# Performance work log

Measured on AMD Instinct MI355X. Metric: run time of the kernel, lower is better.

The kernel has to match this reference:

```python
import jax, jax.numpy as jnp
import numpy as np

EMBED_DIM = 2048
NUM_HEAD = 32
NUM_GROUP = 8
B, S = 2, 2048


def setup_inputs() -> dict:
    key = jax.random.key(0)
    ks = jax.random.split(key, 9)
    D = EMBED_DIM // NUM_HEAD
    kv_dim = NUM_GROUP * D
    s = 0.02
    return {
        "x": jax.random.normal(ks[0], (B, S, EMBED_DIM), dtype=jnp.float32),
        "wq_w": jax.random.normal(ks[1], (EMBED_DIM, EMBED_DIM), dtype=jnp.float32) * s,
        "wq_b": jnp.zeros((EMBED_DIM,), dtype=jnp.float32),
        "wk_w": jax.random.normal(ks[2], (kv_dim, EMBED_DIM), dtype=jnp.float32) * s,
        "wk_b": jnp.zeros((kv_dim,), dtype=jnp.float32),
        "wv_w": jax.random.normal(ks[3], (kv_dim, EMBED_DIM), dtype=jnp.float32) * s,
        "wv_b": jnp.zeros((kv_dim,), dtype=jnp.float32),
        "out_w": jax.random.normal(ks[4], (EMBED_DIM, EMBED_DIM), dtype=jnp.float32) * s,
        "out_b": jnp.zeros((EMBED_DIM,), dtype=jnp.float32),
    }


def reference(x, wq_w, wq_b, wk_w, wk_b, wv_w, wv_b, out_w, out_b):
    b, s, e = x.shape
    H, G = NUM_HEAD, NUM_GROUP
    D = e // H
    r = H // G  # repeat_times
    # projections (torch Linear: x @ W.T + b)
    q = (x @ wq_w.T + wq_b).reshape(b, s, H, D)
    k = (x @ wk_w.T + wk_b).reshape(b, s, G, D)
    v = (x @ wv_w.T + wv_b).reshape(b, s, G, D)
    # faithful to torch.concat([data]*r, dim=2): TILE along head axis
    # (q-head h uses kv-head h mod G)
    k = jnp.concatenate([k] * r, axis=2)  # [b, s, H, D]
    v = jnp.concatenate([v] * r, axis=2)
    # [b, H, s_q, s_k]
    scores = jnp.einsum("bqhd,bkhd->bhqk", q, k) / (D ** 0.5)
    # faithful to F.softmax(dim=1): softmax over the HEAD axis
    attn = jax.nn.softmax(scores, axis=1)
    o = jnp.einsum("bhqk,bkhd->bqhd", attn, v).reshape(b, s, e)
    return o @ out_w.T + out_b
```

## Files before the change

### kernel.cpp

```cpp
#include <hip/hip_runtime.h>


typedef unsigned short u16;
typedef unsigned int u32;
typedef __attribute__((ext_vector_type(8))) __bf16 bf16x8;
typedef __attribute__((ext_vector_type(4))) float f32x4;
typedef __attribute__((ext_vector_type(4))) float float4_t;

#define GLD16(ldsp, gp)                                                  \
  __builtin_amdgcn_global_load_lds(                                      \
      (__attribute__((address_space(1))) void*)(void*)(gp),              \
      (__attribute__((address_space(3))) void*)(void*)(ldsp), 16, 0, 0)

static __device__ __forceinline__ u16 f2bf(float f) {
  union { float f; u32 u; } v; v.f = f;
  u32 u = v.u;
  u32 r = (u + 0x7fffu + ((u >> 16) & 1u)) >> 16;
  return (u16)r;
}

static __device__ __forceinline__ bf16x8 ld8(const u16* p) {
  return *(const bf16x8*)p;
}

#if __has_builtin(__builtin_amdgcn_exp2f)
static __device__ __forceinline__ float fexp2(float x) {
  return __builtin_amdgcn_exp2f(x);
}
#else
static __device__ __forceinline__ float fexp2(float x) {
  float r;
  asm("v_exp_f32 %0, %1\n\ts_nop 0" : "=v"(r) : "v"(x));
  return r;
}
#endif

static __device__ __forceinline__ u32 cvtpk(float a, float b) {
  u32 r;
  asm("v_cvt_pk_bf16_f32 %0, %1, %2" : "=v"(r) : "v"(a), "v"(b));
  return r;
}

static __device__ __forceinline__ void barrier_lgkm() {
  asm volatile("s_waitcnt lgkmcnt(0)" ::: "memory");
  __builtin_amdgcn_s_barrier();
  asm volatile("" ::: "memory");
}

static __device__ __forceinline__ float hsum4(float v) {
  v += __builtin_bit_cast(float, __builtin_amdgcn_update_dpp(
           0, __builtin_bit_cast(int, v), 0x124, 0xf, 0xf, true));
  v += __builtin_bit_cast(float, __builtin_amdgcn_update_dpp(
           0, __builtin_bit_cast(int, v), 0x128, 0xf, 0xf, true));
  return v;
}

__global__ void cvt_all(const float* __restrict__ x, const float* __restrict__ wq,
                        const float* __restrict__ wk, const float* __restrict__ wv,
                        const float* __restrict__ wo, u16* __restrict__ xb,
                        u16* __restrict__ wqb, u16* __restrict__ wkb,
                        u16* __restrict__ wvb, u16* __restrict__ wob) {
  int i = blockIdx.x * blockDim.x + threadIdx.x;
  const int stride = gridDim.x * blockDim.x;
  for (; i < 2359296; i += stride) {
    const float* src;
    u16* dst;
    int j;
    if (i < 1048576)      { src = x;  dst = xb;  j = i; }
    else if (i < 1572864) { src = wq; dst = wqb; j = i - 1048576; }
    else if (i < 1703936) { src = wk; dst = wkb; j = i - 1572864; }
    else if (i < 1835008) { src = wv; dst = wvb; j = i - 1703936; }
    else                  { src = wo; dst = wob; j = i - 1835008; }
    const float4_t* p = (const float4_t*)src + (size_t)j * 2;
    float4_t a = p[0], b = p[1];
    u32 w0 = (u32)f2bf(a[0]) | ((u32)f2bf(a[1]) << 16);
    u32 w1 = (u32)f2bf(a[2]) | ((u32)f2bf(a[3]) << 16);
    u32 w2 = (u32)f2bf(b[0]) | ((u32)f2bf(b[1]) << 16);
    u32 w3 = (u32)f2bf(b[2]) | ((u32)f2bf(b[3]) << 16);
    *(uint4*)(dst + (size_t)j * 8) = make_uint4(w0, w1, w2, w3);
  }
}

template <int MODE>
__global__ __launch_bounds__(256, 2)
void gemm_bt(const u16* __restrict__ A, const u16* __restrict__ Bw,
             const float* __restrict__ bias,
             u16* __restrict__ Cb, float* __restrict__ Cf, int N, float scale) {
  constexpr int K = 2048;
  constexpr int SHSZ = (MODE == 2) ? (128 * 136) : 8192;
  __shared__ u16 sh[SHSZ];
  u16* As = sh;
  u16* Bs = sh + 4096;
  const int tid = threadIdx.x;
  const int lane = tid & 63;
  const int w = tid >> 6;
  const int m0 = blockIdx.y * 128;
  const int n0 = blockIdx.x * 128;
  const int wr = (w >> 1) * 64, wc = (w & 1) * 64;
  const int r15 = lane & 15, kq = lane >> 4;

  f32x4 acc[4][4] = {};

  for (int k0 = 0; k0 < K; k0 += 32) {
#pragma unroll
    for (int i = 0; i < 2; ++i) {
      int c = i * 256 + tid;
      int r = c >> 2, ch = c & 3;
      int sc = (ch ^ (r & 3)) * 8;
      GLD16(&As[c * 8], &A[(size_t)(m0 + r) * K + k0 + sc]);
      GLD16(&Bs[c * 8], &Bw[(size_t)(n0 + r) * K + k0 + sc]);
    }
    __syncthreads();
    bf16x8 af[4], bfr[4];
#pragma unroll
    for (int mt = 0; mt < 4; ++mt) {
      int r = wr + mt * 16 + r15;
      af[mt] = ld8(&As[r * 32 + ((kq ^ (r15 & 3)) * 8)]);
    }
#pragma unroll
    for (int nt = 0; nt < 4; ++nt) {
      int r = wc + nt * 16 + r15;
      bfr[nt] = ld8(&Bs[r * 32 + ((kq ^ (r15 & 3)) * 8)]);
    }
#pragma unroll
    for (int mt = 0; mt < 4; ++mt)
#pragma unroll
      for (int nt = 0; nt < 4; ++nt)
        acc[mt][nt] = __builtin_amdgcn_mfma_f32_16x16x32_bf16(af[mt], bfr[nt], acc[mt][nt], 0, 0, 0);
    __syncthreads();
  }

  if constexpr (MODE == 2) {
#pragma unroll
    for (int mt = 0; mt < 4; ++mt)
#pragma unroll
      for (int nt = 0; nt < 4; ++nt) {
        int col = wc + nt * 16 + r15;
        float bv = bias[n0 + col];
#pragma unroll
        for (int r = 0; r < 4; ++r) {
          int row = wr + mt * 16 + kq * 4 + r;
          sh[col * 136 + row] = f2bf(acc[mt][nt][r] + bv);
        }
      }
    __syncthreads();
    const int m0l = m0 & 2047;
    const int bb = m0 >> 11;
#pragma unroll
    for (int i = 0; i < 8; ++i) {
      int c = i * 256 + tid;
      int cc = c >> 4, so = c & 15;
      int X = cc * 136 + (so >> 2) * 32 + (so & 3) * 4;
      u32 A0 = *(const u32*)&sh[X + 0];
      u32 A1 = *(const u32*)&sh[X + 2];
      u32 B0 = *(const u32*)&sh[X + 16];
      u32 B1 = *(const u32*)&sh[X + 18];
      u32 w0 = __builtin_amdgcn_perm(B0, A0, 0x05040100u);
      u32 w1 = __builtin_amdgcn_perm(B0, A0, 0x07060302u);
      u32 w2 = __builtin_amdgcn_perm(B1, A1, 0x05040100u);
      u32 w3 = __builtin_amdgcn_perm(B1, A1, 0x07060302u);
      *(uint4*)&Cb[(size_t)(bb * 512 + n0 + cc) * 2048 + m0l + so * 8] =
          make_uint4(w0, w1, w2, w3);
    }
  } else {
    const int rb = kq * 4;
#pragma unroll
    for (int mt = 0; mt < 4; ++mt) {
#pragma unroll
      for (int nt = 0; nt < 4; ++nt) {
        int col = n0 + wc + nt * 16 + r15;
        float bv = bias[col];
#pragma unroll
        for (int r = 0; r < 4; ++r) {
          int row = m0 + wr + mt * 16 + rb + r;
          float v = (acc[mt][nt][r] + bv) * scale;
          if constexpr (MODE == 0) Cb[(size_t)row * N + col] = f2bf(v);
          else                     Cf[(size_t)row * N + col] = v;
        }
      }
    }
  }
}

__global__ __launch_bounds__(1024, 4)
void attn_fused(const u16* __restrict__ Q, const u16* __restrict__ Kg,
                const u16* __restrict__ Vt, u16* __restrict__ O) {
  __shared__ float slab[8 * 528];
  __shared__ float rsb[16 * 36];

  const int tid = threadIdx.x;
  const int lane = tid & 63, w = tid >> 6;
  const int g = w & 7, zd = w >> 3;
  const int l15 = lane & 15, kq = lane >> 4;
  const int qr = l15 & 3, hl = l15 >> 2;

  const int xcd = blockIdx.x & 7;
  const int b = xcd >> 2;
  const int q0 = ((((blockIdx.x >> 3) << 2) + (xcd & 3)) << 4);
  const int qbase = q0 + zd * 8;

  const u16* Qb = Q + (size_t)b * 2048 * 2048;
  const u16* Kb = Kg + (size_t)b * 2048 * 512;
  const u16* Vb = Vt + (size_t)b * 512 * 2048;

  bf16x8 qf[2][2];
#pragma unroll
  for (int qq = 0; qq < 2; ++qq)
#pragma unroll
    for (int t = 0; t < 2; ++t)
      qf[qq][t] = ld8(&Qb[(size_t)(qbase + qq * 4 + qr) * 2048 +
                          (g + 8 * hl) * 64 + t * 32 + kq * 8]);

  f32x4 acc[2][4] = {};
  bf16x8 kfA[2][2], kfB[2][2];

#pragma unroll
  for (int ko = 0; ko < 2; ++ko)
#pragma unroll
    for (int t = 0; t < 2; ++t)
      kfA[ko][t] = ld8(&Kb[(size_t)(ko * 16 + l15) * 512 + g * 64 + t * 32 + kq * 8]);

  auto tilestep = [&](int k0, bf16x8 (&kfC)[2][2], bf16x8 (&kfN)[2][2]) {
    f32x4 sc[2][2];
#pragma unroll
    for (int qq = 0; qq < 2; ++qq)
#pragma unroll
      for (int ko = 0; ko < 2; ++ko) {
        f32x4 s = {};
        s = __builtin_amdgcn_mfma_f32_16x16x32_bf16(kfC[ko][0], qf[qq][0], s, 0, 0, 0);
        s = __builtin_amdgcn_mfma_f32_16x16x32_bf16(kfC[ko][1], qf[qq][1], s, 0, 0, 0);
        sc[qq][ko] = s;
      }

    const int kn = (k0 + 32) & 2047;
#pragma unroll
    for (int ko = 0; ko < 2; ++ko)
#pragma unroll
      for (int t = 0; t < 2; ++t)
        kfN[ko][t] = ld8(&Kb[(size_t)(kn + ko * 16 + l15) * 512 + g * 64 + t * 32 + kq * 8]);

    bf16x8 vb[4];
#pragma unroll
    for (int nt = 0; nt < 4; ++nt)
      vb[nt] = ld8(&Vb[(size_t)(g * 64 + nt * 16 + l15) * 2048 + k0 + kq * 8]);

#pragma unroll
    for (int qq = 0; qq < 2; ++qq)
#pragma unroll
      for (int ko = 0; ko < 2; ++ko)
#pragma unroll
        for (int r = 0; r < 4; ++r)
          sc[qq][ko][r] = fexp2(sc[qq][ko][r]);
#pragma unroll
    for (int qq = 0; qq < 2; ++qq)
#pragma unroll
      for (int ko = 0; ko < 2; ++ko)
#pragma unroll
        for (int r = 0; r < 4; ++r) {
          float su = hsum4(sc[qq][ko][r]);
          if (hl == 0)
            slab[g * 528 + (zd * 8 + qq * 4 + qr) * 33 + ko * 16 + kq * 4 + r] = su;
        }

    barrier_lgkm();

    if (tid < 512) {
      int q = tid >> 5, k = tid & 31;
      float s = 0.f;
#pragma unroll
      for (int gg = 0; gg < 8; ++gg) s += slab[gg * 528 + q * 33 + k];
      rsb[q * 36 + k] = __builtin_amdgcn_rcpf(s);
    }

    barrier_lgkm();

#pragma unroll
    for (int qq = 0; qq < 2; ++qq) {
      const int ql = zd * 8 + qq * 4 + qr;
      f32x4 rs0 = *(const f32x4*)&rsb[ql * 36 + kq * 4];
      f32x4 rs1 = *(const f32x4*)&rsb[ql * 36 + 16 + kq * 4];
      u32 paw[4];
#pragma unroll
      for (int r = 0; r < 4; ++r)
        paw[r] = cvtpk(sc[qq][0][r] * rs0[r], sc[qq][1][r] * rs1[r]);
      bf16x8 pa = __builtin_bit_cast(bf16x8, *(uint4*)paw);
#pragma unroll
      for (int nt = 0; nt < 4; ++nt)
        acc[qq][nt] = __builtin_amdgcn_mfma_f32_16x16x32_bf16(pa, vb[nt], acc[qq][nt], 0, 0, 0);
    }
  };

  for (int k0 = 0; k0 < 2048; k0 += 64) {
    tilestep(k0, kfA, kfB);
    tilestep(k0 + 32, kfB, kfA);
  }

#pragma unroll
  for (int qq = 0; qq < 2; ++qq)
#pragma unroll
    for (int nt = 0; nt < 4; ++nt)
#pragma unroll
      for (int r = 0; r < 4; ++r)
        O[(size_t)(b * 2048 + qbase + qq * 4 + r) * 2048 +
          (g + 8 * kq) * 64 + nt * 16 + l15] = f2bf(acc[qq][nt][r]);
}

extern "C" void kernel_launch(void* const* d_in, const int* in_sizes, int n_in,
                              void* d_out, int out_size, void* d_ws, size_t ws_size,
                              hipStream_t stream) {
  (void)in_sizes; (void)n_in; (void)out_size; (void)ws_size;
  const float* x    = (const float*)d_in[0];
  const float* wq_w = (const float*)d_in[1];
  const float* wq_b = (const float*)d_in[2];
  const float* wk_w = (const float*)d_in[3];
  const float* wk_b = (const float*)d_in[4];
  const float* wv_w = (const float*)d_in[5];
  const float* wv_b = (const float*)d_in[6];
  const float* wo_w = (const float*)d_in[7];
  const float* wo_b = (const float*)d_in[8];
  float* out = (float*)d_out;

  char* p = (char*)d_ws;
  u16* xb  = (u16*)p; p += (size_t)4096 * 2048 * 2;
  u16* wqb = (u16*)p; p += (size_t)2048 * 2048 * 2;
  u16* wkb = (u16*)p; p += (size_t)512 * 2048 * 2;
  u16* wvb = (u16*)p; p += (size_t)512 * 2048 * 2;
  u16* wob = (u16*)p; p += (size_t)2048 * 2048 * 2;
  u16* Qb  = (u16*)p; p += (size_t)4096 * 2048 * 2;
  u16* Kb  = (u16*)p; p += (size_t)4096 * 512 * 2;
  u16* Vtb = (u16*)p; p += (size_t)1024 * 2048 * 2;
  u16* Ob  = (u16*)p; p += (size_t)4096 * 2048 * 2;

  hipLaunchKernelGGL(cvt_all, dim3(2048), dim3(256), 0, stream,
                     x, wq_w, wk_w, wv_w, wo_w, xb, wqb, wkb, wvb, wob);

  const float kscale = 0.125f * 1.44269504f;
  hipLaunchKernelGGL((gemm_bt<0>), dim3(16, 32), dim3(256), 0, stream,
                     xb, wqb, wq_b, Qb, (float*)nullptr, 2048, 1.0f);
  hipLaunchKernelGGL((gemm_bt<0>), dim3(4, 32),  dim3(256), 0, stream,
                     xb, wkb, wk_b, Kb, (float*)nullptr, 512, kscale);
  hipLaunchKernelGGL((gemm_bt<2>), dim3(4, 32),  dim3(256), 0, stream,
                     xb, wvb, wv_b, Vtb, (float*)nullptr, 512, 1.0f);

  hipLaunchKernelGGL(attn_fused, dim3(256), dim3(1024), 0, stream, Qb, Kb, Vtb, Ob);

  hipLaunchKernelGGL((gemm_bt<1>), dim3(16, 32), dim3(256), 0, stream,
                     Ob, wob, wo_b, (u16*)nullptr, out, 2048, 1.0f);
}
```

Before: 474.2 us.

## Restructure attention to 512-thread blocks with 64-key tiles per barrier pair

```diff
diff --git a/kernel.cpp b/kernel.cpp
--- a/kernel.cpp
+++ b/kernel.cpp
@@ -11,6 +11,8 @@
   __builtin_amdgcn_global_load_lds(                                      \
       (__attribute__((address_space(1))) void*)(void*)(gp),              \
       (__attribute__((address_space(3))) void*)(void*)(ldsp), 16, 0, 0)
+
+#define MFMA16(a, b, c) __builtin_amdgcn_mfma_f32_16x16x32_bf16(a, b, c, 0, 0, 0)
 
 static __device__ __forceinline__ u16 f2bf(float f) {
   union { float f; u32 u; } v; v.f = f;
@@ -126,7 +128,7 @@
     for (int mt = 0; mt < 4; ++mt)
 #pragma unroll
       for (int nt = 0; nt < 4; ++nt)
-        acc[mt][nt] = __builtin_amdgcn_mfma_f32_16x16x32_bf16(af[mt], bfr[nt], acc[mt][nt], 0, 0, 0);
+        acc[mt][nt] = MFMA16(af[mt], bfr[nt], acc[mt][nt]);
     __syncthreads();
   }
 
@@ -182,22 +184,20 @@
   }
 }
 
-__global__ __launch_bounds__(1024, 4)
+__global__ __launch_bounds__(512, 2)
 void attn_fused(const u16* __restrict__ Q, const u16* __restrict__ Kg,
                 const u16* __restrict__ Vt, u16* __restrict__ O) {
-  __shared__ float slab[8 * 528];
-  __shared__ float rsb[16 * 36];
+  __shared__ float slab[8 * 576];
+  __shared__ float rsb[8 * 72];
 
   const int tid = threadIdx.x;
-  const int lane = tid & 63, w = tid >> 6;
-  const int g = w & 7, zd = w >> 3;
+  const int lane = tid & 63, g = tid >> 6;
   const int l15 = lane & 15, kq = lane >> 4;
   const int qr = l15 & 3, hl = l15 >> 2;
 
   const int xcd = blockIdx.x & 7;
   const int b = xcd >> 2;
-  const int q0 = ((((blockIdx.x >> 3) << 2) + (xcd & 3)) << 4);
-  const int qbase = q0 + zd * 8;
+  const int qbase = ((((blockIdx.x >> 3) << 2) + (xcd & 3)) << 3);
 
   const u16* Qb = Q + (size_t)b * 2048 * 2048;
   const u16* Kb = Kg + (size_t)b * 2048 * 512;
@@ -212,87 +212,85 @@
                           (g + 8 * hl) * 64 + t * 32 + kq * 8]);
 
   f32x4 acc[2][4] = {};
-  bf16x8 kfA[2][2], kfB[2][2];
-
-#pragma unroll
-  for (int ko = 0; ko < 2; ++ko)
+
+  const u16* kbase = &Kb[(size_t)l15 * 512 + g * 64 + kq * 8];
+  const u16* vbase = &Vb[(size_t)(g * 64 + l15) * 2048 + kq * 8];
+
+  for (int k0 = 0; k0 < 2048; k0 += 64) {
+    bf16x8 kf[4][2];
+#pragma unroll
+    for (int ko = 0; ko < 4; ++ko) {
+      kf[ko][0] = ld8(kbase + (size_t)(k0 + ko * 16) * 512);
+      kf[ko][1] = ld8(kbase + (size_t)(k0 + ko * 16) * 512 + 32);
+    }
+    f32x4 sc[2][4];
+#pragma unroll
+    for (int qq = 0; qq < 2; ++qq)
+#pragma unroll
+      for (int ko = 0; ko < 4; ++ko) {
+        f32x4 s = {};
+        s = MFMA16(kf[ko][0], qf[qq][0], s);
+        s = MFMA16(kf[ko][1], qf[qq][1], s);
+        sc[qq][ko] = s;
+      }
+    bf16x8 vb[2][4];
 #pragma unroll
     for (int t = 0; t < 2; ++t)
-      kfA[ko][t] = ld8(&Kb[(size_t)(ko * 16 + l15) * 512 + g * 64 + t * 32 + kq * 8]);
-
-  auto tilestep = [&](int k0, bf16x8 (&kfC)[2][2], bf16x8 (&kfN)[2][2]) {
-    f32x4 sc[2][2];
+#pragma unroll
+      for (int nt = 0; nt < 4; ++nt)
+        vb[t][nt] = ld8(vbase + (size_t)nt * 32768 + k0 + t * 32);
 #pragma unroll
     for (int qq = 0; qq < 2; ++qq)
 #pragma unroll
-      for (int ko = 0; ko < 2; ++ko) {
-        f32x4 s = {};
-        s = __builtin_amdgcn_mfma_f32_16x16x32_bf16(kfC[ko][0], qf[qq][0], s, 0, 0, 0);
-        s = __builtin_amdgcn_mfma_f32_16x16x32_bf16(kfC[ko][1], qf[qq][1], s, 0, 0, 0);
-        sc[qq][ko] = s;
-      }
-
-    const int kn = (k0 + 32) & 2047;
-#pragma unroll
-    for (int ko = 0; ko < 2; ++ko)
-#pragma unroll
-      for (int t = 0; t < 2; ++t)
-        kfN[ko][t] = ld8(&Kb[(size_t)(kn + ko * 16 + l15) * 512 + g * 64 + t * 32 + kq * 8]);
-
-    bf16x8 vb[4];
-#pragma unroll
-    for (int nt = 0; nt < 4; ++nt)
-      vb[nt] = ld8(&Vb[(size_t)(g * 64 + nt * 16 + l15) * 2048 + k0 + kq * 8]);
-
-#pragma unroll
-    for (int qq = 0; qq < 2; ++qq)
-#pragma unroll
-      for (int ko = 0; ko < 2; ++ko)
+      for (int ko = 0; ko < 4; ++ko)
 #pragma unroll
         for (int r = 0; r < 4; ++r)
           sc[qq][ko][r] = fexp2(sc[qq][ko][r]);
 #pragma unroll
     for (int qq = 0; qq < 2; ++qq)
 #pragma unroll
-      for (int ko = 0; ko < 2; ++ko)
-#pragma unroll
-        for (int r = 0; r < 4; ++r) {
-          float su = hsum4(sc[qq][ko][r]);
-          if (hl == 0)
-            slab[g * 528 + (zd * 8 + qq * 4 + qr) * 33 + ko * 16 + kq * 4 + r] = su;
-        }
+      for (int ko = 0; ko < 4; ++ko) {
+        f32x4 u;
+#pragma unroll
+        for (int r = 0; r < 4; ++r) u[r] = hsum4(sc[qq][ko][r]);
+        if (hl == 0)
+          *(f32x4*)&slab[g * 576 + (qq * 4 + qr) * 72 + ko * 16 + kq * 4] = u;
+      }
 
     barrier_lgkm();
 
-    if (tid < 512) {
-      int q = tid >> 5, k = tid & 31;
+    {
+      const int q = tid >> 6, k = tid & 63;
       float s = 0.f;
 #pragma unroll
-      for (int gg = 0; gg < 8; ++gg) s += slab[gg * 528 + q * 33 + k];
-      rsb[q * 36 + k] = __builtin_amdgcn_rcpf(s);
+      for (int gg = 0; gg < 8; ++gg) s += slab[gg * 576 + q * 72 + k];
+      rsb[q * 72 + k] = __builtin_amdgcn_rcpf(s);
     }
 
     barrier_lgkm();
 
 #pragma unroll
     for (int qq = 0; qq < 2; ++qq) {
-      const int ql = zd * 8 + qq * 4 + qr;
-      f32x4 rs0 = *(const f32x4*)&rsb[ql * 36 + kq * 4];
-      f32x4 rs1 = *(const f32x4*)&rsb[ql * 36 + 16 + kq * 4];
+      const float* rq = &rsb[(qq * 4 + qr) * 72 + kq * 4];
+      f32x4 r0 = *(const f32x4*)(rq + 0);
+      f32x4 r1 = *(const f32x4*)(rq + 16);
+      f32x4 r2 = *(const f32x4*)(rq + 32);
+      f32x4 r3 = *(const f32x4*)(rq + 48);
       u32 paw[4];
 #pragma unroll
       for (int r = 0; r < 4; ++r)
-        paw[r] = cvtpk(sc[qq][0][r] * rs0[r], sc[qq][1][r] * rs1[r]);
-      bf16x8 pa = __builtin_bit_cast(bf16x8, *(uint4*)paw);
-#pragma unroll
-      for (int nt = 0; nt < 4; ++nt)
-        acc[qq][nt] = __builtin_amdgcn_mfma_f32_16x16x32_bf16(pa, vb[nt], acc[qq][nt], 0, 0, 0);
-    }
-  };
-
-  for (int k0 = 0; k0 < 2048; k0 += 64) {
-    tilestep(k0, kfA, kfB);
-    tilestep(k0 + 32, kfB, kfA);
+        paw[r] = cvtpk(sc[qq][0][r] * r0[r], sc[qq][1][r] * r1[r]);
+      bf16x8 pa0 = __builtin_bit_cast(bf16x8, *(uint4*)paw);
+#pragma unroll
+      for (int r = 0; r < 4; ++r)
+        paw[r] = cvtpk(sc[qq][2][r] * r2[r], sc[qq][3][r] * r3[r]);
+      bf16x8 pa1 = __builtin_bit_cast(bf16x8, *(uint4*)paw);
+#pragma unroll
+      for (int nt = 0; nt < 4; ++nt) {
+        acc[qq][nt] = MFMA16(pa0, vb[0][nt], acc[qq][nt]);
+        acc[qq][nt] = MFMA16(pa1, vb[1][nt], acc[qq][nt]);
+      }
+    }
   }
 
 #pragma unroll
@@ -342,7 +340,7 @@
   hipLaunchKernelGGL((gemm_bt<2>), dim3(4, 32),  dim3(256), 0, stream,
                      xb, wvb, wv_b, Vtb, (float*)nullptr, 512, 1.0f);
 
-  hipLaunchKernelGGL(attn_fused, dim3(256), dim3(1024), 0, stream, Qb, Kb, Vtb, Ob);
+  hipLaunchKernelGGL(attn_fused, dim3(512), dim3(512), 0, stream, Qb, Kb, Vtb, Ob);
 
   hipLaunchKernelGGL((gemm_bt<1>), dim3(16, 32), dim3(256), 0, stream,
                      Ob, wob, wo_b, (u16*)nullptr, out, 2048, 1.0f);
```

Result: faster. 429.0 us (-9.5%).
